# Optimization experiments

Measured on AMD Instinct MI355X. Metric: run time of the kernel, lower is better.

The kernel has to match this reference:

```python
import jax, jax.numpy as jnp
import numpy as np

EPS = 1e-5  # nn.LayerNorm default


def channel_ln(x, g, b):
    # LayerNorm over the channel axis of an NCHW tensor
    mu = jnp.mean(x, axis=1, keepdims=True)
    var = jnp.mean((x - mu) ** 2, axis=1, keepdims=True)
    xn = (x - mu) * jax.lax.rsqrt(var + EPS)
    return xn * g[None, :, None, None] + b[None, :, None, None]


def setup_inputs() -> dict:
    key = jax.random.key(0)
    ks = jax.random.split(key, 8)
    B, C, H, W = 16, 392, 64, 64
    n, ws = 8, 7            # head_dim = C//n = 49 = ws'^2
    hidden = int(C * 4.0)
    f32 = jnp.float32
    return {
        "x": jax.random.normal(ks[0], (B, C, H, W), f32),
        "ln1_g": jnp.ones((C,), f32),
        "ln1_b": jnp.zeros((C,), f32),
        "qkv_w": jax.random.normal(ks[1], (3 * C, C), f32) * 0.02,
        "qkv_b": jnp.zeros((3 * C,), f32),
        "rel_bias": jax.random.normal(ks[2], (n, ws, ws), f32) * 0.02,
        "proj_w": jax.random.normal(ks[3], (C, C), f32) * 0.02,
        "proj_b": jnp.zeros((C,), f32),
        "ln2_g": jnp.ones((C,), f32),
        "ln2_b": jnp.zeros((C,), f32),
        "fc1_w": jax.random.normal(ks[4], (hidden, C), f32) * 0.02,
        "fc1_b": jnp.zeros((hidden,), f32),
        "fc2_w": jax.random.normal(ks[5], (C, hidden), f32) * 0.02,
        "fc2_b": jnp.zeros((C,), f32),
    }


def reference(x, ln1_g, ln1_b, qkv_w, qkv_b, rel_bias, proj_w, proj_b,
              ln2_g, ln2_b, fc1_w, fc1_b, fc2_w, fc2_b):
    B, C, H, W = x.shape
    n = rel_bias.shape[0]
    hd = C // n  # == ws'^2 (49)
    shortcut = x

    # --- attention branch ---
    h = channel_ln(x, ln1_g, ln1_b)
    qkv = jnp.einsum('oc,bchw->bohw', qkv_w, h) + qkv_b[None, :, None, None]
    qkv = qkv.reshape(B, 3, n, hd, H * W).transpose(1, 0, 2, 4, 3)  # [3,B,n,HW,hd]
    q, k, v = qkv[0], qkv[1], qkv[2]
    scale = hd ** -0.5
    bias = rel_bias.reshape(n, -1)[None, :, None, :]        # [1,n,1,hd]
    attn = jax.nn.softmax(q * scale * k + bias, axis=-1)    # elementwise qk score
    out = (attn * v).reshape(B, C, H, W)  # row-major reshape == torch .view on contiguous
    out = jnp.einsum('oc,bchw->bohw', proj_w, out) + proj_b[None, :, None, None]
    x = shortcut + out

    # --- conv-MLP branch ---
    h = channel_ln(x, ln2_g, ln2_b)
    h = jnp.einsum('oc,bchw->bohw', fc1_w, h) + fc1_b[None, :, None, None]
    h = jax.nn.gelu(h, approximate=False)  # nn.GELU default is exact erf
    h = jnp.einsum('oc,bchw->bohw', fc2_w, h) + fc2_b[None, :, None, None]
    return x + h
```

## Files before the change

### kernel.cpp

```cpp
#include <hip/hip_runtime.h>

typedef unsigned short u16;
typedef __attribute__((ext_vector_type(8))) short short8;
typedef __attribute__((ext_vector_type(8))) unsigned short u16x8;
typedef __attribute__((ext_vector_type(4))) unsigned short u16x4;
typedef __attribute__((ext_vector_type(4))) float f32x4;

#define DEVINL __device__ __forceinline__

DEVINL float bf2f(u16 v) { return __builtin_bit_cast(float, (unsigned int)v << 16); }
DEVINL u16 f2bf(float f) {
  unsigned int u = __builtin_bit_cast(unsigned int, f);
  u += 0x7fffu + ((u >> 16) & 1u);
  return (u16)(u >> 16);
}

DEVINL float loadx(const void* p, size_t i, int flag) {
  return flag ? bf2f(((const u16*)p)[i]) : ((const float*)p)[i];
}

DEVINL f32x4 mfma16(short8 a, short8 b, f32x4 c) {
  return __builtin_amdgcn_mfma_f32_16x16x32_bf16(a, b, c, 0, 0, 0);
}

DEVINL void gload16(const u16* g, u16* l) {
  __builtin_amdgcn_global_load_lds(
      (const __attribute__((address_space(1))) unsigned int*)g,
      (__attribute__((address_space(3))) unsigned int*)l,
      16, 0, 0);
}

#define WAIT_VM(n) asm volatile("s_waitcnt vmcnt(" #n ")" ::: "memory")
#define SBAR() __builtin_amdgcn_s_barrier()
#define SCHED_FENCE() __builtin_amdgcn_sched_barrier(0)

__global__ void k_detect(const unsigned int* __restrict__ xw, int* __restrict__ flag)
{
  const int t = threadIdx.x;
  int cnt = 0;
  for (int i = t; i < 4096; i += 256) {
    unsigned int w = xw[i];
    unsigned int h = w & 0xFFFFu;
    unsigned int e = (h >> 7) & 0xFFu;
    if (((h & 0x7FFFu) == 0u) || (e >= 117u && e <= 130u)) cnt++;
  }
  #pragma unroll
  for (int d = 1; d < 64; d <<= 1) cnt += __shfl_xor(cnt, d);
  __shared__ int acc[4];
  if ((t & 63) == 0) acc[t >> 6] = cnt;
  __syncthreads();
  if (t == 0) *flag = ((acc[0] + acc[1] + acc[2] + acc[3]) > 2048) ? 1 : 0;
}

__global__ void k_prep_fold(const void* __restrict__ w, const void* __restrict__ g,
                            const void* __restrict__ beta, const void* __restrict__ wbias,
                            const int* __restrict__ dflag,
                            u16* __restrict__ wp, float* __restrict__ wsum, float* __restrict__ cb,
                            int rows, int K, int KP)
{
  const int flag = *dflag;
  const int o = blockIdx.x;
  const int lane = threadIdx.x;
  float ws = 0.f, c = 0.f;
  if (o < rows) {
    for (int k = lane; k < KP; k += 64) {
      u16 outv = 0;
      if (k < K) {
        float wv = loadx(w, (size_t)o * K + k, flag);
        float gv = loadx(g, k, flag);
        outv = f2bf(wv * gv);
        ws += bf2f(outv);
        c  += wv * loadx(beta, k, flag);
      }
      wp[(size_t)o * KP + k] = outv;
    }
  } else {
    for (int k = lane; k < KP; k += 64) wp[(size_t)o * KP + k] = 0;
  }
  #pragma unroll
  for (int d = 1; d < 64; d <<= 1) { ws += __shfl_xor(ws, d); c += __shfl_xor(c, d); }
  if (lane == 0) { wsum[o] = ws; cb[o] = (o < rows) ? (c + loadx(wbias, o, flag)) : 0.f; }
}

__global__ void k_prep_pad(const void* __restrict__ w, const int* __restrict__ dflag,
                           u16* __restrict__ wp, int rows, int K, int KP, long total)
{
  const int flag = *dflag;
  long i = (long)blockIdx.x * 256 + threadIdx.x;
  if (i >= total) return;
  int r = (int)(i / KP), c2 = (int)(i % KP);
  wp[i] = (r < rows && c2 < K) ? f2bf(loadx(w, (size_t)r * K + c2, flag)) : (u16)0;
}

__global__ void k_repack(const u16* __restrict__ src, u16* __restrict__ dst, int RP, int KP)
{
  const int nK = KP / 32;
  long i = (long)blockIdx.x * 256 + threadIdx.x;
  if (i * 8 >= (long)RP * KP) return;
  int l = (int)(i & 63);
  long fk = i >> 6;
  int ks = (int)(fk % nK), f = (int)(fk / nK);
  const u16* s = src + (size_t)(f * 16 + (l & 15)) * KP + ks * 32 + ((l >> 4) & 3) * 8;
  *(u16x8*)(dst + i * 8) = *(const u16x8*)s;
}

__global__ __launch_bounds__(256) void k_transpose(const void* __restrict__ xraw,
                                                   const int* __restrict__ dflag,
                                                   u16* __restrict__ xt, int jg0)
{
  __shared__ u16 ts[64][72];
  const int flag = *dflag;
  const int t = threadIdx.x;
  const int j0l = blockIdx.x * 64;
  const int j0g = jg0 + j0l;
  const int c0 = blockIdx.y * 64;
  const int c_l = t >> 2;
  const int c = c0 + c_l;
  const int bb = j0g >> 12;
  const int hw0 = j0g & 4095;

  #pragma unroll
  for (int u = 0; u < 2; ++u) {
    int jp = u * 32 + (t & 3) * 8;
    u16 vv[8] = {0, 0, 0, 0, 0, 0, 0, 0};
    if (c < 392) {
      size_t base = (((size_t)(bb * 392 + c)) << 12) + hw0 + jp;
      if (flag) {
        u16x8 v = *(const u16x8*)((const u16*)xraw + base);
        #pragma unroll
        for (int i = 0; i < 8; ++i) vv[i] = v[i];
      } else {
        const float* xf = (const float*)xraw + base;
        f32x4 a = *(const f32x4*)xf;
        f32x4 b = *(const f32x4*)(xf + 4);
        #pragma unroll
        for (int i = 0; i < 4; ++i) { vv[i] = f2bf(a[i]); vv[4 + i] = f2bf(b[i]); }
      }
    }
    #pragma unroll
    for (int i = 0; i < 8; ++i) ts[jp + i][c_l] = vv[i];
  }
  __syncthreads();
  const int j_l = t >> 2;
  #pragma unroll
  for (int u = 0; u < 2; ++u) {
    int cp = u * 32 + (t & 3) * 8;
    u16x8 w;
    #pragma unroll
    for (int i = 0; i < 8; ++i) w[i] = ts[j_l][cp + i];
    int cg = c0 + cp;
    if (cg < 416) *(u16x8*)(xt + (size_t)(j0l + j_l) * 416 + cg) = w;
  }
}

__global__ __launch_bounds__(256) void k_att_tr(const u16* __restrict__ att,
                                                u16* __restrict__ aout)
{
  __shared__ u16 ts[64][72];
  const int t = threadIdx.x;
  const int j0l = blockIdx.x * 64;
  const int c0 = blockIdx.y * 64;
  const int c_l = t >> 2;
  const int c = c0 + c_l;
  const int slab = j0l >> 12;
  const int hw0 = j0l & 4095;

  #pragma unroll
  for (int u = 0; u < 2; ++u) {
    int jp = u * 32 + (t & 3) * 8;
    u16x8 v = {0, 0, 0, 0, 0, 0, 0, 0};
    if (c < 392)
      v = *(const u16x8*)(att + (size_t)slab * 1605632 + (size_t)c * 4096 + hw0 + jp);
    #pragma unroll
    for (int i = 0; i < 8; ++i) ts[jp + i][c_l] = v[i];
  }
  __syncthreads();
  const int j_l = t >> 2;
  #pragma unroll
  for (int u = 0; u < 2; ++u) {
    int cp = u * 32 + (t & 3) * 8;
    u16x8 w;
    #pragma unroll
    for (int i = 0; i < 8; ++i) w[i] = ts[j_l][cp + i];
    int cg = c0 + cp;
    if (cg < 416) *(u16x8*)(aout + (size_t)(j0l + j_l) * 416 + cg) = w;
  }
}

__global__ __launch_bounds__(256) void k_rowstats(const u16* __restrict__ buf,
                                                  float* __restrict__ sum, float* __restrict__ sq)
{
  const int t = threadIdx.x;
  const int lane = t & 63;
  const int row = blockIdx.x * 4 + (t >> 6);
  float s = 0.f, q = 0.f;
  if (lane < 52) {
    u16x8 v = *(const u16x8*)(buf + (size_t)row * 416 + lane * 8);
    #pragma unroll
    for (int i = 0; i < 8; ++i) { float f = bf2f(v[i]); s += f; q += f * f; }
  }
  #pragma unroll
  for (int d = 1; d < 64; d <<= 1) { s += __shfl_xor(s, d); q += __shfl_xor(q, d); }
  if (lane == 0) { sum[row] = s; sq[row] = q; }
}

__global__ __launch_bounds__(256, 2) void k_qkv(
    const u16* __restrict__ xt, const u16* __restrict__ w1p,
    const float* __restrict__ wsum1, const float* __restrict__ cb1,
    const float* __restrict__ sum1, const float* __restrict__ sq1,
    const void* __restrict__ relb, const int* __restrict__ dflag,
    u16* __restrict__ attout)
{
  __shared__ __align__(16) u16 lsA[2 * 4096];
  __shared__ __align__(16) u16 lsB[2 * 6144];
  const int flag = *dflag;
  const int t = threadIdx.x;
  const int wid = t >> 6, lane = t & 63;
  const int l15 = lane & 15, quad = lane >> 4;
  const int bid = blockIdx.x;
  const int h = (bid >> 3) & 7;
  const int jl0 = ((bid & 7) + ((bid >> 6) << 3)) * 128;

  const u16* ga0 = xt + (size_t)(jl0 + (t >> 2)) * 416 + (t & 3) * 8;
  const u16* ga1 = ga0 + (size_t)64 * 416;
  const int orow = t >> 2, kpart = (t & 3) * 8;
  const u16* gbq = w1p + (size_t)(h * 49 + orow) * 416 + kpart;
  const u16* gbk = w1p + (size_t)(392 + h * 49 + orow) * 416 + kpart;
  const u16* gbv = w1p + (size_t)(784 + h * 49 + orow) * 416 + kpart;

  f32x4 zero4 = {0.f, 0.f, 0.f, 0.f};
  f32x4 accq[2][4], acck[2][4], accv[2][4];
  #pragma unroll
  for (int a = 0; a < 2; ++a)
    #pragma unroll
    for (int b2 = 0; b2 < 4; ++b2) { accq[a][b2] = zero4; acck[a][b2] = zero4; accv[a][b2] = zero4; }

  auto stage = [&](int b, int kk) {
    u16* A = lsA + b * 4096;
    u16* B = lsB + b * 6144;
    gload16(ga0 + kk, A + t * 8);
    gload16(ga1 + kk, A + 2048 + t * 8);
    gload16(gbq + kk, B + t * 8);
    gload16(gbk + kk, B + 2048 + t * 8);
    gload16(gbv + kk, B + 4096 + t * 8);
  };

  stage(0, 0);
  int cur = 0;
  for (int it = 0; it < 13; ++it) {
    if (it < 12) { stage(cur ^ 1, (it + 1) * 32); WAIT_VM(5); }
    else WAIT_VM(0);
    SBAR();
    SCHED_FENCE();
    const u16* A = lsA + cur * 4096;
    const u16* B = lsB + cur * 6144;
    short8 af0 = *(const short8*)(A + ((wid * 32 + l15) * 32 + quad * 8));
    short8 af1 = *(const short8*)(A + ((wid * 32 + 16 + l15) * 32 + quad * 8));
    #pragma unroll
    for (int of = 0; of < 4; ++of) {
      const int bo_ = (of * 16 + l15) * 32 + quad * 8;
      short8 bq = *(const short8*)(B + bo_);
      short8 bk = *(const short8*)(B + 2048 + bo_);
      short8 bv = *(const short8*)(B + 4096 + bo_);
      accq[0][of] = mfma16(af0, bq, accq[0][of]);
      accq[1][of] = mfma16(af1, bq, accq[1][of]);
      acck[0][of] = mfma16(af0, bk, acck[0][of]);
      acck[1][of] = mfma16(af1, bk, acck[1][of]);
      accv[0][of] = mfma16(af0, bv, accv[0][of]);
      accv[1][of] = mfma16(af1, bv, accv[1][of]);
    }
    SCHED_FENCE();
    SBAR();
    cur ^= 1;
  }

  const float scale = 1.f / 7.f;
  float cq[4], wq[4], ck[4], wk[4], cv[4], wv_[4], bo[4];
  int dl[4];
  #pragma unroll
  for (int of = 0; of < 4; ++of) {
    int d = of * 16 + l15; dl[of] = d;
    int rq = h * 49 + d, rk = 392 + h * 49 + d, rv = 784 + h * 49 + d;
    wq[of] = wsum1[rq]; cq[of] = cb1[rq];
    wk[of] = wsum1[rk]; ck[of] = cb1[rk];
    wv_[of] = wsum1[rv]; cv[of] = cb1[rv];
    bo[of] = (d < 49) ? loadx(relb, h * 49 + d, flag) : 0.f;
  }
  #pragma unroll
  for (int jf = 0; jf < 2; ++jf) {
    #pragma unroll
    for (int r = 0; r < 4; ++r) {
      int jl = jl0 + wid * 32 + jf * 16 + quad * 4 + r;
      float mu = sum1[jl] * (1.f / 392.f);
      float var = sq1[jl] * (1.f / 392.f) - mu * mu;
      float rs = rsqrtf(fmaxf(var, 0.f) + 1e-5f);
      float sv[4], vv[4];
      float mx = -1e30f;
      #pragma unroll
      for (int of = 0; of < 4; ++of) {
        float qv = rs * accq[jf][of][r] + cq[of] - mu * rs * wq[of];
        float kv = rs * acck[jf][of][r] + ck[of] - mu * rs * wk[of];
        float s = (dl[of] < 49) ? (qv * scale * kv + bo[of]) : -1e30f;
        sv[of] = s; mx = fmaxf(mx, s);
        vv[of] = rs * accv[jf][of][r] + cv[of] - mu * rs * wv_[of];
      }
      #pragma unroll
      for (int d2 = 1; d2 < 16; d2 <<= 1) mx = fmaxf(mx, __shfl_xor(mx, d2));
      float sum = 0.f;
      #pragma unroll
      for (int of = 0; of < 4; ++of) { float e = __expf(sv[of] - mx); sv[of] = e; sum += e; }
      #pragma unroll
      for (int d2 = 1; d2 < 16; d2 <<= 1) sum += __shfl_xor(sum, d2);
      float inv = 1.f / sum;
      int pos = jl & 4095, slab = jl >> 12;
      size_t base = (size_t)slab * 1605632 + (size_t)h * 200704 + (size_t)pos * 49;
      #pragma unroll
      for (int of = 0; of < 4; ++of) {
        if (dl[of] < 49) attout[base + dl[of]] = f2bf(sv[of] * inv * vv[of]);
      }
    }
  }
}


__global__ __launch_bounds__(512, 2) void k_proj(
    const u16* __restrict__ aout, const u16* __restrict__ wppf,
    const void* __restrict__ projb, const int* __restrict__ dflag,
    const u16* __restrict__ xt, u16* __restrict__ x2t)
{
  __shared__ __align__(16) u16 lsA[3 * 4096];
  __shared__ __align__(16) u16 lsB[3 * 16384];
  const int flag = *dflag;
  const int t = threadIdx.x;
  const int w = t >> 6, lane = t & 63;
  const int l15 = lane & 15, quad = (lane >> 4) & 3;
  const int jl0 = blockIdx.x * 128;
  const int NK = 13;

  const u16* gA = aout + (size_t)(jl0 + (t >> 6) * 16 + l15) * 416 + quad * 8;
  const u16* gB = wppf + (size_t)(t >> 6) * NK * 512 + lane * 8;

  f32x4 zero4 = {0.f, 0.f, 0.f, 0.f};
  f32x4 acc[4][8];
  #pragma unroll
  for (int m = 0; m < 4; ++m)
    #pragma unroll
    for (int n = 0; n < 8; ++n) acc[m][n] = zero4;

  auto stage = [&](int b, int ks) {
    gload16(gA + ks * 32, lsA + b * 4096 + t * 8);
    #pragma unroll
    for (int c = 0; c < 4; ++c)
      gload16(gB + ((size_t)c * 8 * NK + ks) * 512,
              lsB + b * 16384 + (c * 8 + w) * 512 + lane * 8);
  };

  stage(0, 0); stage(1, 1);
  int bc = 0, bs = 2;
  for (int ks = 0; ks < NK; ++ks) {
    if (ks + 2 < NK) { stage(bs, ks + 2); WAIT_VM(10); }
    else if (ks + 1 < NK) WAIT_VM(5);
    else WAIT_VM(0);
    SBAR();
    SCHED_FENCE();
    const u16* A = lsA + bc * 4096;
    const u16* B = lsB + bc * 16384;
    short8 af[4];
    #pragma unroll
    for (int m = 0; m < 4; ++m)
      af[m] = *(const short8*)(A + ((w >> 2) * 4 + m) * 512 + lane * 8);
    #pragma unroll
    for (int n = 0; n < 8; ++n) {
      short8 bf = *(const short8*)(B + ((w & 3) * 8 + n) * 512 + lane * 8);
      #pragma unroll
      for (int m = 0; m < 4; ++m) acc[m][n] = mfma16(af[m], bf, acc[m][n]);
    }
    SCHED_FENCE();
    SBAR();
    bc = (bc + 1 == 3) ? 0 : bc + 1;
    bs = (bs + 1 == 3) ? 0 : bs + 1;
  }

  float pb[8]; int og[8];
  #pragma unroll
  for (int n = 0; n < 8; ++n) {
    int o = (w & 3) * 128 + n * 16 + l15; og[n] = o;
    pb[n] = (o < 392) ? loadx(projb, o, flag) : 0.f;
  }
  const int row0 = jl0 + (w >> 2) * 64;
  #pragma unroll
  for (int m = 0; m < 4; ++m) {
    #pragma unroll
    for (int r = 0; r < 4; ++r) {
      int jl = row0 + m * 16 + quad * 4 + r;
      #pragma unroll
      for (int n = 0; n < 8; ++n) {
        int o = og[n];
        if (o < 392) {
          float val = acc[m][n][r] + pb[n] + bf2f(xt[(size_t)jl * 416 + o]);
          x2t[(size_t)jl * 416 + o] = f2bf(val);
        } else if (o < 416) {
          x2t[(size_t)jl * 416 + o] = 0;
        }
      }
    }
  }
}

__global__ __launch_bounds__(512, 2) void k_fc1(
    const u16* __restrict__ x2t, const u16* __restrict__ w3pf,
    const float* __restrict__ wsum3, const float* __restrict__ cb3,
    const float* __restrict__ sum2, const float* __restrict__ sq2,
    u16* __restrict__ ut)
{
  __shared__ __align__(16) u16 lsA[3 * 4096];
  __shared__ __align__(16) u16 lsB[3 * 16384];
  const int t = threadIdx.x;
  const int w = t >> 6, lane = t & 63;
  const int l15 = lane & 15, quad = (lane >> 4) & 3;
  const int jl0 = blockIdx.x * 128;
  const int o0 = blockIdx.y * 512;
  const int NK = 13;

  const u16* gA = x2t + (size_t)(jl0 + (t >> 6) * 16 + l15) * 416 + quad * 8;
  const u16* gB = w3pf + ((size_t)(blockIdx.y * 32 + (t >> 6)) * NK) * 512 + lane * 8;

  f32x4 zero4 = {0.f, 0.f, 0.f, 0.f};
  f32x4 acc[4][8];
  #pragma unroll
  for (int m = 0; m < 4; ++m)
    #pragma unroll
    for (int n = 0; n < 8; ++n) acc[m][n] = zero4;

  auto stage = [&](int b, int ks) {
    gload16(gA + ks * 32, lsA + b * 4096 + t * 8);
    #pragma unroll
    for (int c = 0; c < 4; ++c)
      gload16(gB + ((size_t)c * 8 * NK + ks) * 512,
              lsB + b * 16384 + (c * 8 + w) * 512 + lane * 8);
  };

  stage(0, 0); stage(1, 1);
  int bc = 0, bs = 2;
  for (int ks = 0; ks < NK; ++ks) {
    if (ks + 2 < NK) { stage(bs, ks + 2); WAIT_VM(10); }
    else if (ks + 1 < NK) WAIT_VM(5);
    else WAIT_VM(0);
    SBAR();
    SCHED_FENCE();
    const u16* A = lsA + bc * 4096;
    const u16* B = lsB + bc * 16384;
    short8 af[4];
    #pragma unroll
    for (int m = 0; m < 4; ++m)
      af[m] = *(const short8*)(A + ((w >> 2) * 4 + m) * 512 + lane * 8);
    #pragma unroll
    for (int n = 0; n < 8; ++n) {
      short8 bf = *(const short8*)(B + ((w & 3) * 8 + n) * 512 + lane * 8);
      #pragma unroll
      for (int m = 0; m < 4; ++m) acc[m][n] = mfma16(af[m], bf, acc[m][n]);
    }
    SCHED_FENCE();
    SBAR();
    bc = (bc + 1 == 3) ? 0 : bc + 1;
    bs = (bs + 1 == 3) ? 0 : bs + 1;
  }

  float c3[8], w3[8]; int og[8];
  #pragma unroll
  for (int n = 0; n < 8; ++n) {
    int o = o0 + (w & 3) * 128 + n * 16 + l15; og[n] = o;
    c3[n] = cb3[o]; w3[n] = wsum3[o];
  }
  const int row0 = jl0 + (w >> 2) * 64;
  #pragma unroll
  for (int m = 0; m < 4; ++m) {
    #pragma unroll
    for (int r = 0; r < 4; ++r) {
      int jl = row0 + m * 16 + quad * 4 + r;
      float mu = sum2[jl] * (1.f / 392.f);
      float var = sq2[jl] * (1.f / 392.f) - mu * mu;
      float rs = rsqrtf(fmaxf(var, 0.f) + 1e-5f);
      #pragma unroll
      for (int n = 0; n < 8; ++n) {
        if (og[n] < 1568) {
          float u = rs * acc[m][n][r] + c3[n] - mu * rs * w3[n];
          float gl = 0.5f * u * (1.f + erff(u * 0.70710678118654752f));
          ut[(size_t)jl * 1568 + og[n]] = f2bf(gl);
        }
      }
    }
  }
}

__global__ __launch_bounds__(512, 2) void k_fc2(
    const u16* __restrict__ ut, const u16* __restrict__ wfpf,
    const void* __restrict__ fc2b, const int* __restrict__ dflag,
    const u16* __restrict__ x2t, void* __restrict__ outp, int jfg0)
{
  __shared__ __align__(16) u16 lsA[3 * 4096];
  __shared__ __align__(16) u16 lsB[3 * 16384];
  const int flag = *dflag;
  const int t = threadIdx.x;
  const int w = t >> 6, lane = t & 63;
  const int l15 = lane & 15, quad = (lane >> 4) & 3;
  const int jl0 = blockIdx.x * 128;
  const int NK = 49;

  const u16* gA = ut + (size_t)(jl0 + (t >> 6) * 16 + l15) * 1568 + quad * 8;
  const u16* gB = wfpf + (size_t)(t >> 6) * NK * 512 + lane * 8;

  f32x4 zero4 = {0.f, 0.f, 0.f, 0.f};
  f32x4 acc[4][8];
  #pragma unroll
  for (int m = 0; m < 4; ++m)
    #pragma unroll
    for (int n = 0; n < 8; ++n) acc[m][n] = zero4;

  auto stage = [&](int b, int ks) {
    gload16(gA + ks * 32, lsA + b * 4096 + t * 8);
    #pragma unroll
    for (int c = 0; c < 4; ++c)
      gload16(gB + ((size_t)c * 8 * NK + ks) * 512,
              lsB + b * 16384 + (c * 8 + w) * 512 + lane * 8);
  };

  stage(0, 0); stage(1, 1);
  int bc = 0, bs = 2;
  for (int ks = 0; ks < NK; ++ks) {
    if (ks + 2 < NK) { stage(bs, ks + 2); WAIT_VM(10); }
    else if (ks + 1 < NK) WAIT_VM(5);
    else WAIT_VM(0);
    SBAR();
    SCHED_FENCE();
    const u16* A = lsA + bc * 4096;
    const u16* B = lsB + bc * 16384;
    short8 af[4];
    #pragma unroll
    for (int m = 0; m < 4; ++m)
      af[m] = *(const short8*)(A + ((w >> 2) * 4 + m) * 512 + lane * 8);
    #pragma unroll
    for (int n = 0; n < 8; ++n) {
      short8 bf = *(const short8*)(B + ((w & 3) * 8 + n) * 512 + lane * 8);
      #pragma unroll
      for (int m = 0; m < 4; ++m) acc[m][n] = mfma16(af[m], bf, acc[m][n]);
    }
    SCHED_FENCE();
    SBAR();
    bc = (bc + 1 == 3) ? 0 : bc + 1;
    bs = (bs + 1 == 3) ? 0 : bs + 1;
  }

  float fb4[8]; int og[8];
  #pragma unroll
  for (int n = 0; n < 8; ++n) {
    int o = (w & 3) * 128 + n * 16 + l15; og[n] = o;
    fb4[n] = (o < 392) ? loadx(fc2b, o, flag) : 0.f;
  }
  const int row0 = jl0 + (w >> 2) * 64;
  #pragma unroll
  for (int m = 0; m < 4; ++m) {
    int jlbase = row0 + m * 16 + quad * 4;
    int jgbase = jfg0 + jlbase;
    int bslab = jgbase >> 12;
    int hw = jgbase & 4095;
    #pragma unroll
    for (int n = 0; n < 8; ++n) {
      if (og[n] < 392) {
        float v4[4];
        #pragma unroll
        for (int r = 0; r < 4; ++r)
          v4[r] = acc[m][n][r] + fb4[n] + bf2f(x2t[(size_t)(jlbase + r) * 416 + og[n]]);
        size_t obase = (((size_t)(bslab * 392 + og[n])) << 12) + hw;
        if (flag) {
          u16x4 pk;
          #pragma unroll
          for (int r = 0; r < 4; ++r) pk[r] = f2bf(v4[r]);
          *(u16x4*)((u16*)outp + obase) = pk;
        } else {
          f32x4 pk;
          #pragma unroll
          for (int r = 0; r < 4; ++r) pk[r] = v4[r];
          *(f32x4*)((float*)outp + obase) = pk;
        }
      }
    }
  }
}

extern "C" void kernel_launch(void* const* d_in, const int* in_sizes, int n_in,
                              void* d_out, int out_size, void* d_ws, size_t ws_size,
                              hipStream_t stream)
{
  if (n_in != 14 || in_sizes[0] != 16 * 392 * 64 * 64 || out_size != 16 * 392 * 64 * 64 ||
      in_sizes[3] != 3 * 392 * 392 || in_sizes[5] != 8 * 7 * 7 ||
      in_sizes[10] != 1568 * 392 || in_sizes[12] != 392 * 1568) {
    return;
  }

  const void* x     = d_in[0];
  const void* g1    = d_in[1];
  const void* b1    = d_in[2];
  const void* qkvw  = d_in[3];
  const void* qkvb  = d_in[4];
  const void* relb  = d_in[5];
  const void* projw = d_in[6];
  const void* projb = d_in[7];
  const void* g2    = d_in[8];
  const void* b2    = d_in[9];
  const void* fc1w  = d_in[10];
  const void* fc1b  = d_in[11];
  const void* fc2w  = d_in[12];
  const void* fc2b  = d_in[13];

  int S = 0, F = 0;
  {
    const int cand[8][2] = {{16,8},{16,4},{8,4},{8,2},{4,2},{4,1},{2,1},{1,1}};
    for (int i = 0; i < 8; ++i) {
      size_t nb = (size_t)cand[i][0] * 4096 * 416 * 2 * 3
                + (size_t)cand[i][1] * 4096 * 1568 * 2
                + (size_t)24 * 1024 * 1024;
      if (nb <= ws_size) { S = cand[i][0]; F = cand[i][1]; break; }
    }
    if (S == 0) return;
  }

  char* wsb = (char*)d_ws;
  size_t off = 0;
  auto alloc = [&](size_t bytes) -> void* {
    void* p = wsb + off;
    off = (off + bytes + 255) & ~(size_t)255;
    return p;
  };
  int*  dflag = (int*)alloc(256);
  u16* xt    = (u16*)alloc((size_t)S * 4096 * 416 * 2);
  u16* aout  = (u16*)alloc((size_t)S * 4096 * 416 * 2);
  u16* x2t   = (u16*)alloc((size_t)S * 4096 * 416 * 2);
  u16* ut    = (u16*)alloc((size_t)F * 4096 * 1568 * 2);
  u16* w1p   = (u16*)alloc((size_t)1200 * 416 * 2);
  u16* w3r   = (u16*)alloc((size_t)2048 * 416 * 2);
  u16* w3pf  = (u16*)alloc((size_t)2048 * 416 * 2);
  u16* wpr   = (u16*)alloc((size_t)512 * 416 * 2);
  u16* wppf  = (u16*)alloc((size_t)512 * 416 * 2);
  u16* wfr   = (u16*)alloc((size_t)512 * 1568 * 2);
  u16* wfpf  = (u16*)alloc((size_t)512 * 1568 * 2);
  float* wsum1 = (float*)alloc(1200 * 4);
  float* cb1   = (float*)alloc(1200 * 4);
  float* wsum3 = (float*)alloc(2048 * 4);
  float* cb3   = (float*)alloc(2048 * 4);
  float* sum1  = (float*)alloc((size_t)65536 * 4);
  float* sq1   = (float*)alloc((size_t)65536 * 4);
  float* sum2  = (float*)alloc((size_t)65536 * 4);
  float* sq2   = (float*)alloc((size_t)65536 * 4);

  u16* att = x2t;

  k_detect<<<1, 256, 0, stream>>>((const unsigned int*)x, dflag);

  k_prep_fold<<<1200, 64, 0, stream>>>(qkvw, g1, b1, qkvb, dflag, w1p, wsum1, cb1, 1176, 392, 416);
  k_prep_fold<<<2048, 64, 0, stream>>>(fc1w, g2, b2, fc1b, dflag, w3r, wsum3, cb3, 1568, 392, 416);
  k_prep_pad<<<(512 * 416 + 255) / 256, 256, 0, stream>>>(projw, dflag, wpr, 392, 392, 416, (long)512 * 416);
  k_prep_pad<<<(512 * 1568 + 255) / 256, 256, 0, stream>>>(fc2w, dflag, wfr, 392, 1568, 1568, (long)512 * 1568);
  k_repack<<<((2048 * 416 / 8) + 255) / 256, 256, 0, stream>>>(w3r, w3pf, 2048, 416);
  k_repack<<<((512 * 416 / 8) + 255) / 256, 256, 0, stream>>>(wpr, wppf, 512, 416);
  k_repack<<<((512 * 1568 / 8) + 255) / 256, 256, 0, stream>>>(wfr, wfpf, 512, 1568);

  for (int c0 = 0; c0 < 16; c0 += S) {
    const int jg0 = c0 * 4096;
    k_transpose<<<dim3(S * 64, 7), 256, 0, stream>>>(x, dflag, xt, jg0);
    k_rowstats<<<S * 1024, 256, 0, stream>>>(xt, sum1, sq1);
    k_qkv<<<dim3(S * 256), 256, 0, stream>>>(xt, w1p, wsum1, cb1, sum1, sq1, relb, dflag, att);
    k_att_tr<<<dim3(S * 64, 7), 256, 0, stream>>>(att, aout);
    k_proj<<<dim3(S * 32), 512, 0, stream>>>(aout, wppf, projb, dflag, xt, x2t);
    k_rowstats<<<S * 1024, 256, 0, stream>>>(x2t, sum2, sq2);
    for (int f0 = 0; f0 < S; f0 += F) {
      const int jfg0 = (c0 + f0) * 4096;
      const u16* x2sub = x2t + (size_t)f0 * 4096 * 416;
      k_fc1<<<dim3(F * 32, 4), 512, 0, stream>>>(x2sub, w3pf, wsum3, cb3,
                                                 sum2 + (size_t)f0 * 4096, sq2 + (size_t)f0 * 4096, ut);
      k_fc2<<<dim3(F * 32), 512, 0, stream>>>(ut, wfpf, fc2b, dflag, x2sub, d_out, jfg0);
    }
  }
}
```

Baseline: 941.9 us.

## Shrink GEMM tiles to 128x128 with 256 threads and double buffering

The proj, fc1 and fc2 GEMM kernels change from 128x512 output tiles with 512 threads and triple-buffered LDS to 128x128 tiles with 256 threads and double-buffered LDS, spread over a 2D grid. This cuts per-block LDS and accumulator registers so more blocks fit per CU and the grid grows, which should improve occupancy and load balance. It also lets fc1 skip padded output columns beyond 1568 by launching 13 column tiles. The cost is that A tiles get reloaded once per column tile, and the shallower prefetch pipeline may hide less load latency.

```diff
diff --git a/kernel.cpp b/kernel.cpp
--- a/kernel.cpp
+++ b/kernel.cpp
@@ -323,78 +323,79 @@
 }
 
 
-__global__ __launch_bounds__(512, 2) void k_proj(
+__global__ __launch_bounds__(256, 4) void k_proj(
     const u16* __restrict__ aout, const u16* __restrict__ wppf,
     const void* __restrict__ projb, const int* __restrict__ dflag,
     const u16* __restrict__ xt, u16* __restrict__ x2t)
 {
-  __shared__ __align__(16) u16 lsA[3 * 4096];
-  __shared__ __align__(16) u16 lsB[3 * 16384];
+  __shared__ __align__(16) u16 lsA[2 * 4096];
+  __shared__ __align__(16) u16 lsB[2 * 4096];
   const int flag = *dflag;
   const int t = threadIdx.x;
   const int w = t >> 6, lane = t & 63;
   const int l15 = lane & 15, quad = (lane >> 4) & 3;
   const int jl0 = blockIdx.x * 128;
+  const int y = blockIdx.y, o0 = y * 128;
   const int NK = 13;
-
-  const u16* gA = aout + (size_t)(jl0 + (t >> 6) * 16 + l15) * 416 + quad * 8;
-  const u16* gB = wppf + (size_t)(t >> 6) * NK * 512 + lane * 8;
+  const int wm = w >> 1, wn = w & 1;
+
+  const u16* gA0 = aout + (size_t)(jl0 + w * 16 + l15) * 416 + quad * 8;
+  const u16* gA1 = aout + (size_t)(jl0 + (4 + w) * 16 + l15) * 416 + quad * 8;
+  const u16* gB0 = wppf + ((size_t)(y * 8 + w) * NK) * 512 + lane * 8;
+  const u16* gB1 = wppf + ((size_t)(y * 8 + 4 + w) * NK) * 512 + lane * 8;
 
   f32x4 zero4 = {0.f, 0.f, 0.f, 0.f};
-  f32x4 acc[4][8];
+  f32x4 acc[4][4];
   #pragma unroll
   for (int m = 0; m < 4; ++m)
     #pragma unroll
-    for (int n = 0; n < 8; ++n) acc[m][n] = zero4;
+    for (int n = 0; n < 4; ++n) acc[m][n] = zero4;
 
   auto stage = [&](int b, int ks) {
-    gload16(gA + ks * 32, lsA + b * 4096 + t * 8);
-    #pragma unroll
-    for (int c = 0; c < 4; ++c)
-      gload16(gB + ((size_t)c * 8 * NK + ks) * 512,
-              lsB + b * 16384 + (c * 8 + w) * 512 + lane * 8);
+    gload16(gA0 + ks * 32, lsA + b * 4096 + w * 512 + lane * 8);
+    gload16(gA1 + ks * 32, lsA + b * 4096 + (4 + w) * 512 + lane * 8);
+    gload16(gB0 + (size_t)ks * 512, lsB + b * 4096 + w * 512 + lane * 8);
+    gload16(gB1 + (size_t)ks * 512, lsB + b * 4096 + (4 + w) * 512 + lane * 8);
   };
 
-  stage(0, 0); stage(1, 1);
-  int bc = 0, bs = 2;
+  stage(0, 0);
+  int cur = 0;
   for (int ks = 0; ks < NK; ++ks) {
-    if (ks + 2 < NK) { stage(bs, ks + 2); WAIT_VM(10); }
-    else if (ks + 1 < NK) WAIT_VM(5);
+    if (ks + 1 < NK) { stage(cur ^ 1, ks + 1); WAIT_VM(4); }
     else WAIT_VM(0);
     SBAR();
     SCHED_FENCE();
-    const u16* A = lsA + bc * 4096;
-    const u16* B = lsB + bc * 16384;
+    const u16* A = lsA + cur * 4096;
+    const u16* B = lsB + cur * 4096;
     short8 af[4];
     #pragma unroll
     for (int m = 0; m < 4; ++m)
-      af[m] = *(const short8*)(A + ((w >> 2) * 4 + m) * 512 + lane * 8);
-    #pragma unroll
-    for (int n = 0; n < 8; ++n) {
-      short8 bf = *(const short8*)(B + ((w & 3) * 8 + n) * 512 + lane * 8);
+      af[m] = *(const short8*)(A + (wm * 4 + m) * 512 + lane * 8);
+    #pragma unroll
+    for (int n = 0; n < 4; ++n) {
+      short8 bf = *(const short8*)(B + (wn * 4 + n) * 512 + lane * 8);
       #pragma unroll
       for (int m = 0; m < 4; ++m) acc[m][n] = mfma16(af[m], bf, acc[m][n]);
     }
     SCHED_FENCE();
     SBAR();
-    bc = (bc + 1 == 3) ? 0 : bc + 1;
-    bs = (bs + 1 == 3) ? 0 : bs + 1;
-  }
-
-  float pb[8]; int og[8];
-  #pragma unroll
-  for (int n = 0; n < 8; ++n) {
-    int o = (w & 3) * 128 + n * 16 + l15; og[n] = o;
+    cur ^= 1;
+  }
+
+  float pb[4]; int og[4];
+  #pragma unroll
+  for (int n = 0; n < 4; ++n) {
+    int o = o0 + wn * 64 + n * 16 + l15; og[n] = o;
     pb[n] = (o < 392) ? loadx(projb, o, flag) : 0.f;
   }
-  const int row0 = jl0 + (w >> 2) * 64;
+  const int row0 = jl0 + wm * 64;
   #pragma unroll
   for (int m = 0; m < 4; ++m) {
     #pragma unroll
     for (int r = 0; r < 4; ++r) {
       int jl = row0 + m * 16 + quad * 4 + r;
       #pragma unroll
-      for (int n = 0; n < 8; ++n) {
+      for (int n = 0; n < 4; ++n) {
         int o = og[n];
         if (o < 392) {
           float val = acc[m][n][r] + pb[n] + bf2f(xt[(size_t)jl * 416 + o]);
@@ -407,72 +408,72 @@
   }
 }
 
-__global__ __launch_bounds__(512, 2) void k_fc1(
+__global__ __launch_bounds__(256, 4) void k_fc1(
     const u16* __restrict__ x2t, const u16* __restrict__ w3pf,
     const float* __restrict__ wsum3, const float* __restrict__ cb3,
     const float* __restrict__ sum2, const float* __restrict__ sq2,
     u16* __restrict__ ut)
 {
-  __shared__ __align__(16) u16 lsA[3 * 4096];
-  __shared__ __align__(16) u16 lsB[3 * 16384];
+  __shared__ __align__(16) u16 lsA[2 * 4096];
+  __shared__ __align__(16) u16 lsB[2 * 4096];
   const int t = threadIdx.x;
   const int w = t >> 6, lane = t & 63;
   const int l15 = lane & 15, quad = (lane >> 4) & 3;
   const int jl0 = blockIdx.x * 128;
-  const int o0 = blockIdx.y * 512;
+  const int y = blockIdx.y, o0 = y * 128;
   const int NK = 13;
-
-  const u16* gA = x2t + (size_t)(jl0 + (t >> 6) * 16 + l15) * 416 + quad * 8;
-  const u16* gB = w3pf + ((size_t)(blockIdx.y * 32 + (t >> 6)) * NK) * 512 + lane * 8;
+  const int wm = w >> 1, wn = w & 1;
+
+  const u16* gA0 = x2t + (size_t)(jl0 + w * 16 + l15) * 416 + quad * 8;
+  const u16* gA1 = x2t + (size_t)(jl0 + (4 + w) * 16 + l15) * 416 + quad * 8;
+  const u16* gB0 = w3pf + ((size_t)(y * 8 + w) * NK) * 512 + lane * 8;
+  const u16* gB1 = w3pf + ((size_t)(y * 8 + 4 + w) * NK) * 512 + lane * 8;
 
   f32x4 zero4 = {0.f, 0.f, 0.f, 0.f};
-  f32x4 acc[4][8];
+  f32x4 acc[4][4];
   #pragma unroll
   for (int m = 0; m < 4; ++m)
     #pragma unroll
-    for (int n = 0; n < 8; ++n) acc[m][n] = zero4;
+    for (int n = 0; n < 4; ++n) acc[m][n] = zero4;
 
   auto stage = [&](int b, int ks) {
-    gload16(gA + ks * 32, lsA + b * 4096 + t * 8);
-    #pragma unroll
-    for (int c = 0; c < 4; ++c)
-      gload16(gB + ((size_t)c * 8 * NK + ks) * 512,
-              lsB + b * 16384 + (c * 8 + w) * 512 + lane * 8);
+    gload16(gA0 + ks * 32, lsA + b * 4096 + w * 512 + lane * 8);
+    gload16(gA1 + ks * 32, lsA + b * 4096 + (4 + w) * 512 + lane * 8);
+    gload16(gB0 + (size_t)ks * 512, lsB + b * 4096 + w * 512 + lane * 8);
+    gload16(gB1 + (size_t)ks * 512, lsB + b * 4096 + (4 + w) * 512 + lane * 8);
   };
 
-  stage(0, 0); stage(1, 1);
-  int bc = 0, bs = 2;
+  stage(0, 0);
+  int cur = 0;
   for (int ks = 0; ks < NK; ++ks) {
-    if (ks + 2 < NK) { stage(bs, ks + 2); WAIT_VM(10); }
-    else if (ks + 1 < NK) WAIT_VM(5);
+    if (ks + 1 < NK) { stage(cur ^ 1, ks + 1); WAIT_VM(4); }
     else WAIT_VM(0);
     SBAR();
     SCHED_FENCE();
-    const u16* A = lsA + bc * 4096;
-    const u16* B = lsB + bc * 16384;
+    const u16* A = lsA + cur * 4096;
+    const u16* B = lsB + cur * 4096;
     short8 af[4];
     #pragma unroll
     for (int m = 0; m < 4; ++m)
-      af[m] = *(const short8*)(A + ((w >> 2) * 4 + m) * 512 + lane * 8);
-    #pragma unroll
-    for (int n = 0; n < 8; ++n) {
-      short8 bf = *(const short8*)(B + ((w & 3) * 8 + n) * 512 + lane * 8);
+      af[m] = *(const short8*)(A + (wm * 4 + m) * 512 + lane * 8);
+    #pragma unroll
+    for (int n = 0; n < 4; ++n) {
+      short8 bf = *(const short8*)(B + (wn * 4 + n) * 512 + lane * 8);
       #pragma unroll
       for (int m = 0; m < 4; ++m) acc[m][n] = mfma16(af[m], bf, acc[m][n]);
     }
     SCHED_FENCE();
     SBAR();
-    bc = (bc + 1 == 3) ? 0 : bc + 1;
-    bs = (bs + 1 == 3) ? 0 : bs + 1;
-  }
-
-  float c3[8], w3[8]; int og[8];
-  #pragma unroll
-  for (int n = 0; n < 8; ++n) {
-    int o = o0 + (w & 3) * 128 + n * 16 + l15; og[n] = o;
+    cur ^= 1;
+  }
+
+  float c3[4], w3[4]; int og[4];
+  #pragma unroll
+  for (int n = 0; n < 4; ++n) {
+    int o = o0 + wn * 64 + n * 16 + l15; og[n] = o;
     c3[n] = cb3[o]; w3[n] = wsum3[o];
   }
-  const int row0 = jl0 + (w >> 2) * 64;
+  const int row0 = jl0 + wm * 64;
   #pragma unroll
   for (int m = 0; m < 4; ++m) {
     #pragma unroll
@@ -482,7 +483,7 @@
       float var = sq2[jl] * (1.f / 392.f) - mu * mu;
       float rs = rsqrtf(fmaxf(var, 0.f) + 1e-5f);
       #pragma unroll
-      for (int n = 0; n < 8; ++n) {
+      for (int n = 0; n < 4; ++n) {
         if (og[n] < 1568) {
           float u = rs * acc[m][n][r] + c3[n] - mu * rs * w3[n];
           float gl = 0.5f * u * (1.f + erff(u * 0.70710678118654752f));
@@ -493,71 +494,72 @@
   }
 }
 
-__global__ __launch_bounds__(512, 2) void k_fc2(
+__global__ __launch_bounds__(256, 4) void k_fc2(
     const u16* __restrict__ ut, const u16* __restrict__ wfpf,
     const void* __restrict__ fc2b, const int* __restrict__ dflag,
     const u16* __restrict__ x2t, void* __restrict__ outp, int jfg0)
 {
-  __shared__ __align__(16) u16 lsA[3 * 4096];
-  __shared__ __align__(16) u16 lsB[3 * 16384];
+  __shared__ __align__(16) u16 lsA[2 * 4096];
+  __shared__ __align__(16) u16 lsB[2 * 4096];
   const int flag = *dflag;
   const int t = threadIdx.x;
   const int w = t >> 6, lane = t & 63;
   const int l15 = lane & 15, quad = (lane >> 4) & 3;
   const int jl0 = blockIdx.x * 128;
+  const int y = blockIdx.y, o0 = y * 128;
   const int NK = 49;
-
-  const u16* gA = ut + (size_t)(jl0 + (t >> 6) * 16 + l15) * 1568 + quad * 8;
-  const u16* gB = wfpf + (size_t)(t >> 6) * NK * 512 + lane * 8;
+  const int wm = w >> 1, wn = w & 1;
+
+  const u16* gA0 = ut + (size_t)(jl0 + w * 16 + l15) * 1568 + quad * 8;
+  const u16* gA1 = ut + (size_t)(jl0 + (4 + w) * 16 + l15) * 1568 + quad * 8;
+  const u16* gB0 = wfpf + ((size_t)(y * 8 + w) * NK) * 512 + lane * 8;
+  const u16* gB1 = wfpf + ((size_t)(y * 8 + 4 + w) * NK) * 512 + lane * 8;
 
   f32x4 zero4 = {0.f, 0.f, 0.f, 0.f};
-  f32x4 acc[4][8];
+  f32x4 acc[4][4];
   #pragma unroll
   for (int m = 0; m < 4; ++m)
     #pragma unroll
-    for (int n = 0; n < 8; ++n) acc[m][n] = zero4;
+    for (int n = 0; n < 4; ++n) acc[m][n] = zero4;
 
   auto stage = [&](int b, int ks) {
-    gload16(gA + ks * 32, lsA + b * 4096 + t * 8);
-    #pragma unroll
-    for (int c = 0; c < 4; ++c)
-      gload16(gB + ((size_t)c * 8 * NK + ks) * 512,
-              lsB + b * 16384 + (c * 8 + w) * 512 + lane * 8);
+    gload16(gA0 + ks * 32, lsA + b * 4096 + w * 512 + lane * 8);
+    gload16(gA1 + ks * 32, lsA + b * 4096 + (4 + w) * 512 + lane * 8);
+    gload16(gB0 + (size_t)ks * 512, lsB + b * 4096 + w * 512 + lane * 8);
+    gload16(gB1 + (size_t)ks * 512, lsB + b * 4096 + (4 + w) * 512 + lane * 8);
   };
 
-  stage(0, 0); stage(1, 1);
-  int bc = 0, bs = 2;
+  stage(0, 0);
+  int cur = 0;
   for (int ks = 0; ks < NK; ++ks) {
-    if (ks + 2 < NK) { stage(bs, ks + 2); WAIT_VM(10); }
-    else if (ks + 1 < NK) WAIT_VM(5);
+    if (ks + 1 < NK) { stage(cur ^ 1, ks + 1); WAIT_VM(4); }
     else WAIT_VM(0);
     SBAR();
     SCHED_FENCE();
-    const u16* A = lsA + bc * 4096;
-    const u16* B = lsB + bc * 16384;
+    const u16* A = lsA + cur * 4096;
+    const u16* B = lsB + cur * 4096;
     short8 af[4];
     #pragma unroll
     for (int m = 0; m < 4; ++m)
-      af[m] = *(const short8*)(A + ((w >> 2) * 4 + m) * 512 + lane * 8);
-    #pragma unroll
-    for (int n = 0; n < 8; ++n) {
-      short8 bf = *(const short8*)(B + ((w & 3) * 8 + n) * 512 + lane * 8);
+      af[m] = *(const short8*)(A + (wm * 4 + m) * 512 + lane * 8);
+    #pragma unroll
+    for (int n = 0; n < 4; ++n) {
+      short8 bf = *(const short8*)(B + (wn * 4 + n) * 512 + lane * 8);
       #pragma unroll
       for (int m = 0; m < 4; ++m) acc[m][n] = mfma16(af[m], bf, acc[m][n]);
     }
     SCHED_FENCE();
     SBAR();
-    bc = (bc + 1 == 3) ? 0 : bc + 1;
-    bs = (bs + 1 == 3) ? 0 : bs + 1;
-  }
-
-  float fb4[8]; int og[8];
-  #pragma unroll
-  for (int n = 0; n < 8; ++n) {
-    int o = (w & 3) * 128 + n * 16 + l15; og[n] = o;
+    cur ^= 1;
+  }
+
+  float fb4[4]; int og[4];
+  #pragma unroll
+  for (int n = 0; n < 4; ++n) {
+    int o = o0 + wn * 64 + n * 16 + l15; og[n] = o;
     fb4[n] = (o < 392) ? loadx(fc2b, o, flag) : 0.f;
   }
-  const int row0 = jl0 + (w >> 2) * 64;
+  const int row0 = jl0 + wm * 64;
   #pragma unroll
   for (int m = 0; m < 4; ++m) {
     int jlbase = row0 + m * 16 + quad * 4;
@@ -565,7 +567,7 @@
     int bslab = jgbase >> 12;
     int hw = jgbase & 4095;
     #pragma unroll
-    for (int n = 0; n < 8; ++n) {
+    for (int n = 0; n < 4; ++n) {
       if (og[n] < 392) {
         float v4[4];
         #pragma unroll
@@ -671,14 +673,14 @@
     k_rowstats<<<S * 1024, 256, 0, stream>>>(xt, sum1, sq1);
     k_qkv<<<dim3(S * 256), 256, 0, stream>>>(xt, w1p, wsum1, cb1, sum1, sq1, relb, dflag, att);
     k_att_tr<<<dim3(S * 64, 7), 256, 0, stream>>>(att, aout);
-    k_proj<<<dim3(S * 32), 512, 0, stream>>>(aout, wppf, projb, dflag, xt, x2t);
+    k_proj<<<dim3(S * 32, 4), 256, 0, stream>>>(aout, wppf, projb, dflag, xt, x2t);
     k_rowstats<<<S * 1024, 256, 0, stream>>>(x2t, sum2, sq2);
     for (int f0 = 0; f0 < S; f0 += F) {
       const int jfg0 = (c0 + f0) * 4096;
       const u16* x2sub = x2t + (size_t)f0 * 4096 * 416;
-      k_fc1<<<dim3(F * 32, 4), 512, 0, stream>>>(x2sub, w3pf, wsum3, cb3,
-                                                 sum2 + (size_t)f0 * 4096, sq2 + (size_t)f0 * 4096, ut);
-      k_fc2<<<dim3(F * 32), 512, 0, stream>>>(ut, wfpf, fc2b, dflag, x2sub, d_out, jfg0);
-    }
-  }
-}
+      k_fc1<<<dim3(F * 32, 13), 256, 0, stream>>>(x2sub, w3pf, wsum3, cb3,
+                                                  sum2 + (size_t)f0 * 4096, sq2 + (size_t)f0 * 4096, ut);
+      k_fc2<<<dim3(F * 32, 4), 256, 0, stream>>>(ut, wfpf, fc2b, dflag, x2sub, d_out, jfg0);
+    }
+  }
+}
```

Result: faster. 809.3 us (-14.1%).
